# Performance work log

Measured on AMD Instinct MI355X. Metric: run time of the kernel, lower is better.

The kernel has to match this reference:

```python
import jax, jax.numpy as jnp
import numpy as np

B, T, U, V = 8, 128, 64, 512  # batch, enc frames, label length, vocab
U1 = U + 1
BLANK = 0


def setup_inputs() -> dict:
    key = jax.random.key(0)
    k1, k2, k3, k4, k5 = jax.random.split(key, 5)
    trans_acts = jax.random.normal(k1, (B, T, V), jnp.float32)
    pred_acts = jax.random.normal(k2, (B, U1, V), jnp.float32)
    labels = jax.random.randint(k3, (B, U), 1, V).astype(jnp.int32)  # 0 is blank
    act_lens = jax.random.randint(k4, (B,), T // 2, T + 1).astype(jnp.int32)
    label_lens = jax.random.randint(k5, (B,), U // 2, U + 1).astype(jnp.int32)
    return dict(trans_acts=trans_acts, pred_acts=pred_acts, labels=labels,
                act_lens=act_lens, label_lens=label_lens)


def _rnnt_costs(trans_acts, pred_acts, labels, act_lens, label_lens, blank=BLANK):
    # joint log-probs: log_softmax(trans[t] + pred[u]) over vocab -> (B,T,U1,V)
    logits = trans_acts[:, :, None, :] + pred_acts[:, None, :, :]
    logp = jax.nn.log_softmax(logits, axis=-1)
    lp_blank = logp[..., blank]                                    # (B,T,U1)
    # label emission log-prob at (t,u): prob of labels[b,u]        # (B,T,U)
    lp_lab = jnp.take_along_axis(
        logp[:, :, :U, :], labels[:, None, :, None].astype(jnp.int32), axis=-1)[..., 0]

    nb, nu1 = trans_acts.shape[0], pred_acts.shape[1]
    # alpha at t=0: alpha[0,u] = sum_{u'<u} lp_lab[0,u']
    alpha0 = jnp.concatenate(
        [jnp.zeros((nb, 1), logp.dtype), jnp.cumsum(lp_lab[:, 0, :], axis=-1)], axis=1)

    def t_step(alpha_prev, xs):
        blank_prev, lab_cur = xs                 # (B,U1), (B,U)
        a_in = alpha_prev + blank_prev           # vertical (blank) transition

        def u_step(carry, x):
            a, d = x                             # a:(B,) from blank path, d:(B,) label lp
            new = jnp.logaddexp(a, carry + d)
            return new, new

        _, rest = jax.lax.scan(u_step, a_in[:, 0], (a_in[:, 1:].T, lab_cur.T))
        alpha_t = jnp.concatenate([a_in[:, :1], rest.T], axis=1)
        return alpha_t, alpha_t

    xs = (jnp.swapaxes(lp_blank[:, :-1, :], 0, 1),   # blank lp at t-1: (T-1,B,U1)
          jnp.swapaxes(lp_lab[:, 1:, :], 0, 1))      # label lp at t:  (T-1,B,U)
    _, alphas = jax.lax.scan(t_step, alpha0, xs)     # (T-1,B,U1)
    alphas = jnp.concatenate([alpha0[None], alphas], axis=0)  # (T,B,U1)

    b_idx = jnp.arange(nb)
    t_idx = act_lens - 1
    u_idx = label_lens
    ll = alphas[t_idx, b_idx, u_idx] + lp_blank[b_idx, t_idx, u_idx]
    return -ll                                       # per-example cost (B,)


def reference(trans_acts, pred_acts, labels, act_lens, label_lens):
    costs = _rnnt_costs(trans_acts, pred_acts, labels, act_lens, label_lens)
    # size_average=False: return summed cost as a length-1 vector (as torch FloatTensor([sum]))
    return jnp.sum(costs)[None]
```

## Files before the change

### kernel.cpp

```cpp
#include <hip/hip_runtime.h>
#include <math.h>

#define Bn 8
#define Tn 128
#define Un 64
#define U1n 65
#define Vn 512
#define NEG (-1e30f)
#define LOG2E 1.4426950408889634f
#define LN2 0.6931471805599453f
#define EPH 520
#define ETW 516

template <int CTRL>
__device__ __forceinline__ float dpp_mv(float x) {
  return __int_as_float(__builtin_amdgcn_update_dpp(
      __float_as_int(x), __float_as_int(x), CTRL, 0xF, 0xF, false));
}

__device__ __forceinline__ float red_sum64(float m) {
  m += dpp_mv<0xB1>(m);
  m += dpp_mv<0x4E>(m);
  m += dpp_mv<0x141>(m);
  m += dpp_mv<0x140>(m);
  m += __shfl_xor(m, 16);
  m += __shfl_xor(m, 32);
  return m;
}

__device__ __forceinline__ float wave_shr1_fill(float x, float fill) {
  return __int_as_float(__builtin_amdgcn_update_dpp(
      __float_as_int(fill), __float_as_int(x), 0x138, 0xF, 0xF, false));
}

__device__ __forceinline__ float hw_exp2(float x) {
  return __builtin_amdgcn_exp2f(x);
}
__device__ __forceinline__ float hw_log2(float x) {
  return __builtin_amdgcn_logf(x);
}

__device__ __forceinline__ float laddexp2(float a, float b) {
  float mx = fmaxf(a, b), mn = fminf(a, b);
  return mx + hw_log2(1.f + hw_exp2(mn - mx));
}

__device__ __forceinline__ unsigned short f2bf(float x) {
  unsigned u = __float_as_uint(x);
  u += 0x7fffu + ((u >> 16) & 1u);
  return (unsigned short)(u >> 16);
}

__global__ __launch_bounds__(256) void rnnt_dots(
    const float* __restrict__ trans, const float* __restrict__ pred,
    const int* __restrict__ labels, float* __restrict__ lbT,
    float* __restrict__ llT, float* __restrict__ out) {
  __shared__ unsigned short EPh[U1n * EPH];
  __shared__ float ETs[4 * ETW];
  __shared__ float pr0s[U1n];
  __shared__ float prls[Un];
  __shared__ int lbls[Un];

  if (blockIdx.x == 0 && threadIdx.x == 0) out[0] = 0.f;

  int b = blockIdx.x >> 5;
  int chunk = blockIdx.x & 31;
  int tid = threadIdx.x;
  int w = tid >> 6;
  int lane = tid & 63;
  int t = chunk * 4 + w;

  if (tid < U1n) {
    pr0s[tid] = pred[((size_t)b * U1n + tid) * Vn];
    if (tid < Un) {
      int lbl = labels[b * Un + tid];
      lbls[tid] = lbl;
      prls[tid] = pred[((size_t)b * U1n + tid) * Vn + lbl];
    }
  }

  const float4* pred4 = (const float4*)(pred + (size_t)b * U1n * Vn);
#pragma unroll
  for (int k = 0; k < 33; ++k) {
    int idx = tid + k * 256;
    if (idx < U1n * 128) {
      int u = idx >> 7, j = idx & 127;
      float4 pv = pred4[u * 128 + j];
      ushort4 ev;
      ev.x = f2bf(hw_exp2(pv.x * LOG2E));
      ev.y = f2bf(hw_exp2(pv.y * LOG2E));
      ev.z = f2bf(hw_exp2(pv.z * LOG2E));
      ev.w = f2bf(hw_exp2(pv.w * LOG2E));
      *(ushort4*)&EPh[u * EPH + j * 4] = ev;
    }
  }

  const float* trow = trans + ((size_t)b * Tn + t) * Vn;
  const float4* trow4 = (const float4*)trow;
  {
    float4 x0 = trow4[lane], x1 = trow4[lane + 64];
    float4 e0, e1;
    e0.x = hw_exp2(x0.x * LOG2E); e0.y = hw_exp2(x0.y * LOG2E);
    e0.z = hw_exp2(x0.z * LOG2E); e0.w = hw_exp2(x0.w * LOG2E);
    e1.x = hw_exp2(x1.x * LOG2E); e1.y = hw_exp2(x1.y * LOG2E);
    e1.z = hw_exp2(x1.z * LOG2E); e1.w = hw_exp2(x1.w * LOG2E);
    *(float4*)&ETs[w * ETW + lane * 8] = e0;
    *(float4*)&ETs[w * ETW + lane * 8 + 4] = e1;
  }
  __syncthreads();

  int u = lane;
  float ac0 = 0.f, ac1 = 0.f, ac2 = 0.f, ac3 = 0.f;
  int epb = u * EPH, etb = w * ETW;
#pragma unroll 4
  for (int vc = 0; vc < Vn; vc += 8) {
    uint4 ph = *(const uint4*)&EPh[epb + vc];
    float4 etA = *(const float4*)&ETs[etb + vc];
    float4 etB = *(const float4*)&ETs[etb + vc + 4];
    ac0 = fmaf(etA.x, __uint_as_float(ph.x << 16), ac0);
    ac1 = fmaf(etA.y, __uint_as_float(ph.x & 0xffff0000u), ac1);
    ac2 = fmaf(etA.z, __uint_as_float(ph.y << 16), ac2);
    ac3 = fmaf(etA.w, __uint_as_float(ph.y & 0xffff0000u), ac3);
    ac0 = fmaf(etB.x, __uint_as_float(ph.z << 16), ac0);
    ac1 = fmaf(etB.y, __uint_as_float(ph.z & 0xffff0000u), ac1);
    ac2 = fmaf(etB.z, __uint_as_float(ph.w << 16), ac2);
    ac3 = fmaf(etB.w, __uint_as_float(ph.w & 0xffff0000u), ac3);
  }
  float dot = (ac0 + ac2) + (ac1 + ac3);

  float p64;
  {
    uint4 ph = *(const uint4*)&EPh[64 * EPH + lane * 8];
    float4 tA = *(const float4*)&ETs[etb + lane * 8];
    float4 tB = *(const float4*)&ETs[etb + lane * 8 + 4];
    float part = tA.x * __uint_as_float(ph.x << 16) +
                 tA.y * __uint_as_float(ph.x & 0xffff0000u) +
                 tA.z * __uint_as_float(ph.y << 16) +
                 tA.w * __uint_as_float(ph.y & 0xffff0000u) +
                 tB.x * __uint_as_float(ph.z << 16) +
                 tB.y * __uint_as_float(ph.z & 0xffff0000u) +
                 tB.z * __uint_as_float(ph.w << 16) +
                 tB.w * __uint_as_float(ph.w & 0xffff0000u);
    p64 = red_sum64(part);
  }

  float tr0v = trow[0];
  float lse2 = hw_log2(dot);
  lbT[((size_t)b * U1n + u) * Tn + t] = (tr0v + pr0s[u]) * LOG2E - lse2;
  float trl = trow[lbls[u]];
  llT[((size_t)b * Un + u) * Tn + t] = (trl + prls[u]) * LOG2E - lse2;
  if (lane == 0) {
    lbT[((size_t)b * U1n + 64) * Tn + t] =
        (tr0v + pr0s[64]) * LOG2E - hw_log2(p64);
  }
}

__global__ __launch_bounds__(64) void rnnt_alpha(
    const float* __restrict__ lbT, const float* __restrict__ llT,
    const int* __restrict__ act_lens, const int* __restrict__ label_lens,
    float* __restrict__ out) {
  int b = blockIdx.x;
  int l = threadIdx.x;

  const float* LBrow = lbT + ((size_t)b * U1n + l + 1) * Tn;
  const float* LLrow = llT + ((size_t)b * Un + l) * Tn;
  const float* L0row = lbT + (size_t)b * U1n * Tn;

  int ti = act_lens[b] - 1;
  int ui = label_lens[b];
  int s_end = ti + ui;
  bool is_rec = (l == ui - 1);

  float a = NEG, p = 0.f, rec = 0.f;
  float lbB[8], llB[8], l0B[8];
#pragma unroll
  for (int k = 0; k < 8; ++k) {
    lbB[k] = LBrow[k - l - 1];
    llB[k] = LLrow[k - l];
    l0B[k] = L0row[k];
  }

  for (int sb = 0; sb < s_end; sb += 8) {
#pragma unroll
    for (int k = 0; k < 8; ++k) {
      int s = sb + k;
      float lb_t = lbB[k], ll_t = llB[k], l0_t = l0B[k];
      lbB[k] = LBrow[s + 8 - l - 1];
      llB[k] = LLrow[s + 8 - l];
      l0B[k] = L0row[s + 8];

      float nb = wave_shr1_fill(a, p);
      float vert = a + lb_t;
      float horiz = nb + ll_t;
      float an = laddexp2(vert, horiz);
      int t = s - l;
      a = (t >= 0) ? an : NEG;
      p += l0_t;
      if ((t == ti) & is_rec) rec = an;
    }
  }

  float r = __shfl(rec, ui - 1);
  if (l == 0) {
    float lbv = lbT[((size_t)b * U1n + ui) * Tn + ti];
    atomicAdd(out, -(r + lbv) * LN2);
  }
}

extern "C" void kernel_launch(void* const* d_in, const int* in_sizes, int n_in,
                              void* d_out, int out_size, void* d_ws, size_t ws_size,
                              hipStream_t stream) {
  const float* trans = (const float*)d_in[0];
  const float* pred = (const float*)d_in[1];
  const int* labels = (const int*)d_in[2];
  const int* act_lens = (const int*)d_in[3];
  const int* label_lens = (const int*)d_in[4];
  float* out = (float*)d_out;

  float* lbT = (float*)d_ws + 64;
  float* llT = lbT + Bn * U1n * Tn;

  rnnt_dots<<<Bn * 32, 256, 0, stream>>>(trans, pred, labels, lbT, llT, out);
  rnnt_alpha<<<Bn, 64, 0, stream>>>(lbT, llT, act_lens, label_lens, out);
}
```

Before: 26.52 us.

## Fuse dot and alpha kernels via inter-block flags with diagonal-major scratch layout

```diff
diff --git a/kernel.cpp b/kernel.cpp
--- a/kernel.cpp
+++ b/kernel.cpp
@@ -11,6 +11,9 @@
 #define LN2 0.6931471805599453f
 #define EPH 520
 #define ETW 516
+#define SROWS 208
+#define SDSZ (SROWS * 64)
+#define MAGIC 0x5EC0DE5Au
 
 template <int CTRL>
 __device__ __forceinline__ float dpp_mv(float x) {
@@ -51,17 +54,17 @@
   return (unsigned short)(u >> 16);
 }
 
-__global__ __launch_bounds__(256) void rnnt_dots(
+__global__ __launch_bounds__(256) void rnnt_fused(
     const float* __restrict__ trans, const float* __restrict__ pred,
-    const int* __restrict__ labels, float* __restrict__ lbT,
-    float* __restrict__ llT, float* __restrict__ out) {
+    const int* __restrict__ labels, const int* __restrict__ act_lens,
+    const int* __restrict__ label_lens, float* __restrict__ lbD,
+    float* __restrict__ llD, float* __restrict__ l0D,
+    unsigned* __restrict__ dflag, float* __restrict__ out) {
   __shared__ unsigned short EPh[U1n * EPH];
   __shared__ float ETs[4 * ETW];
   __shared__ float pr0s[U1n];
   __shared__ float prls[Un];
   __shared__ int lbls[Un];
-
-  if (blockIdx.x == 0 && threadIdx.x == 0) out[0] = 0.f;
 
   int b = blockIdx.x >> 5;
   int chunk = blockIdx.x & 31;
@@ -69,6 +72,9 @@
   int w = tid >> 6;
   int lane = tid & 63;
   int t = chunk * 4 + w;
+
+  if (blockIdx.x == 0 && tid == 0)
+    __hip_atomic_store(out, 0.f, __ATOMIC_RELEASE, __HIP_MEMORY_SCOPE_AGENT);
 
   if (tid < U1n) {
     pr0s[tid] = pred[((size_t)b * U1n + tid) * Vn];
@@ -146,25 +152,44 @@
 
   float tr0v = trow[0];
   float lse2 = hw_log2(dot);
-  lbT[((size_t)b * U1n + u) * Tn + t] = (tr0v + pr0s[u]) * LOG2E - lse2;
-  float trl = trow[lbls[u]];
-  llT[((size_t)b * Un + u) * Tn + t] = (trl + prls[u]) * LOG2E - lse2;
+  float lbv = (tr0v + pr0s[u]) * LOG2E - lse2;
+  float llv = (trow[lbls[u]] + prls[u]) * LOG2E - lse2;
+
+  float* lbDb = lbD + (size_t)b * SDSZ;
+  float* llDb = llD + (size_t)b * SDSZ;
   if (lane == 0) {
-    lbT[((size_t)b * U1n + 64) * Tn + t] =
-        (tr0v + pr0s[64]) * LOG2E - hw_log2(p64);
-  }
-}
-
-__global__ __launch_bounds__(64) void rnnt_alpha(
-    const float* __restrict__ lbT, const float* __restrict__ llT,
-    const int* __restrict__ act_lens, const int* __restrict__ label_lens,
-    float* __restrict__ out) {
-  int b = blockIdx.x;
-  int l = threadIdx.x;
-
-  const float* LBrow = lbT + ((size_t)b * U1n + l + 1) * Tn;
-  const float* LLrow = llT + ((size_t)b * Un + l) * Tn;
-  const float* L0row = lbT + (size_t)b * U1n * Tn;
+    l0D[b * 256 + t] = lbv;
+    lbDb[(t + 64) * 64 + 63] = (tr0v + pr0s[64]) * LOG2E - hw_log2(p64);
+  } else {
+    lbDb[(t + lane) * 64 + (lane - 1)] = lbv;
+  }
+  llDb[(t + lane) * 64 + lane] = llv;
+  if (t == 0) lbDb[lane * 64 + lane] = NEG;
+
+  __syncthreads();
+
+  if (chunk != 0) {
+    if (tid == 0)
+      __hip_atomic_store(&dflag[b * 32 + chunk], MAGIC, __ATOMIC_RELEASE,
+                         __HIP_MEMORY_SCOPE_AGENT);
+    return;
+  }
+  if (tid >= 64) return;
+  int l = lane;
+
+  {
+    int idx = b * 32 + ((l < 31) ? l + 1 : 31);
+    while (true) {
+      unsigned v = __hip_atomic_load(&dflag[idx], __ATOMIC_ACQUIRE,
+                                     __HIP_MEMORY_SCOPE_AGENT);
+      if (!__any(v != MAGIC)) break;
+      __builtin_amdgcn_s_sleep(1);
+    }
+  }
+
+  const float* LBd = lbD + (size_t)b * SDSZ;
+  const float* LLd = llD + (size_t)b * SDSZ;
+  const float* L0d = l0D + b * 256;
 
   int ti = act_lens[b] - 1;
   int ui = label_lens[b];
@@ -172,38 +197,38 @@
   bool is_rec = (l == ui - 1);
 
   float a = NEG, p = 0.f, rec = 0.f;
-  float lbB[8], llB[8], l0B[8];
+  float lbB[16], llB[16], l0B[16];
 #pragma unroll
-  for (int k = 0; k < 8; ++k) {
-    lbB[k] = LBrow[k - l - 1];
-    llB[k] = LLrow[k - l];
-    l0B[k] = L0row[k];
-  }
-
-  for (int sb = 0; sb < s_end; sb += 8) {
+  for (int k = 0; k < 16; ++k) {
+    lbB[k] = LBd[k * 64 + l];
+    llB[k] = LLd[k * 64 + l];
+    l0B[k] = L0d[k];
+  }
+
+  for (int sb = 0; sb < s_end; sb += 16) {
 #pragma unroll
-    for (int k = 0; k < 8; ++k) {
+    for (int k = 0; k < 16; ++k) {
       int s = sb + k;
       float lb_t = lbB[k], ll_t = llB[k], l0_t = l0B[k];
-      lbB[k] = LBrow[s + 8 - l - 1];
-      llB[k] = LLrow[s + 8 - l];
-      l0B[k] = L0row[s + 8];
+      lbB[k] = LBd[(s + 16) * 64 + l];
+      llB[k] = LLd[(s + 16) * 64 + l];
+      l0B[k] = L0d[s + 16];
 
       float nb = wave_shr1_fill(a, p);
       float vert = a + lb_t;
       float horiz = nb + ll_t;
       float an = laddexp2(vert, horiz);
-      int t = s - l;
-      a = (t >= 0) ? an : NEG;
+      int tt = s - l;
+      a = (tt >= 0) ? an : NEG;
       p += l0_t;
-      if ((t == ti) & is_rec) rec = an;
+      if ((tt == ti) & is_rec) rec = an;
     }
   }
 
   float r = __shfl(rec, ui - 1);
   if (l == 0) {
-    float lbv = lbT[((size_t)b * U1n + ui) * Tn + ti];
-    atomicAdd(out, -(r + lbv) * LN2);
+    float lbf = LBd[s_end * 64 + (ui - 1)];
+    atomicAdd(out, -(r + lbf) * LN2);
   }
 }
 
@@ -217,9 +242,12 @@
   const int* label_lens = (const int*)d_in[4];
   float* out = (float*)d_out;
 
-  float* lbT = (float*)d_ws + 64;
-  float* llT = lbT + Bn * U1n * Tn;
-
-  rnnt_dots<<<Bn * 32, 256, 0, stream>>>(trans, pred, labels, lbT, llT, out);
-  rnnt_alpha<<<Bn, 64, 0, stream>>>(lbT, llT, act_lens, label_lens, out);
-}
+  float* lbD = (float*)d_ws;
+  float* llD = lbD + Bn * SDSZ;
+  float* l0D = llD + Bn * SDSZ;
+  unsigned* dflag = (unsigned*)(l0D + Bn * 256);
+
+  rnnt_fused<<<Bn * 32, 256, 0, stream>>>(trans, pred, labels, act_lens,
+                                          label_lens, lbD, llD, l0D, dflag,
+                                          out);
+}
```

New measurement: 31.99 us. +20.6%, slower.
